# Kernel optimization log

Measured on AMD Instinct MI355X. Metric: run time of the kernel, lower is better.

## Reference

```python
import jax, jax.numpy as jnp
import numpy as np

H, W, V = 32, 64, 13
B, C_IN = 8, 256
RADIUS = 6371.0 * 1000.0
NUM_LAT = H + 2
_j = np.arange(1, NUM_LAT - 1, dtype=np.float64)
_LATS = (90.0 - _j * 180.0 / (NUM_LAT - 1)) * np.pi / 180.0  # [32] radians
PIXEL_X = jnp.asarray(2.0 * np.pi * RADIUS * np.cos(_LATS) / W, dtype=jnp.float32).reshape(1, 1, H, 1)
PIXEL_Y = np.float32(np.pi * RADIUS / (H + 1))
_DZ = np.array([50, 50, 50, 50, 50, 75, 100, 100, 100, 125, 112, 75, 75], dtype=np.float32)
PIXEL_Z = jnp.asarray(_DZ).reshape(1, V, 1, 1)
PRESSURE = jnp.asarray([50, 100, 150, 200, 250, 300, 400, 500, 600, 700, 850, 925, 1000], dtype=jnp.float32).reshape(1, V, 1, 1)
M_Z = jnp.asarray(np.tril(np.ones((V, V), dtype=np.float32)) * _DZ[None, :])  # lower-tri integration matrix
LAT_GRID = jnp.asarray(_LATS, dtype=jnp.float32).reshape(1, 1, H, 1)

OMEGA, L_V, R_GAS, C_P, R_D = 7.29e-5, 2.5e6, 8.314, 1005.0, 287.0
DIFF_RATIO, DT, K_H, K_V = 0.05, 300.0, 15.0, 0.1
SIGMA, EMIS, PTHRESH = 5.67e-8, 0.7, 0.8
sg = jax.lax.stop_gradient


def d_x(f):  # periodic 4th-order diff along W, kernel [1,-8,0,8,-1]/12
    g = (jnp.roll(f, 2, 3) - 8.0 * jnp.roll(f, 1, 3) + 8.0 * jnp.roll(f, -1, 3) - jnp.roll(f, -2, 3)) / 12.0
    return g / PIXEL_X


def d_y(f):  # replicate-block padding along H, kernel [-1,8,0,-8,1]/12
    p = jnp.concatenate([f[:, :, :2], f, f[:, :, -2:]], axis=2)
    g = (-p[:, :, :-4] + 8.0 * p[:, :, 1:-3] - 8.0 * p[:, :, 3:-1] + p[:, :, 4:]) / 12.0
    return g / PIXEL_Y


def d_z(f):  # replicate-block padding along level dim (axis 1)
    p = jnp.concatenate([f[:, :2], f, f[:, -2:]], axis=1)
    g = (-p[:, :-4] + 8.0 * p[:, 1:-3] - 8.0 * p[:, 3:-1] + p[:, 4:]) / 12.0
    return g / PIXEL_Z


def integral_z(f):
    return jnp.einsum('ij,bjhw->bihw', M_Z, f)


def conv3x3(x, w, b):
    y = jax.lax.conv_general_dilated(x, w, (1, 1), ((1, 1), (1, 1)), dimension_numbers=('NCHW', 'OIHW', 'NCHW'))
    return y + b[None, :, None, None]


def batchnorm(x, g, b, eps=1e-5):  # training-mode BN (batch statistics)
    m = x.mean(axis=(0, 2, 3), keepdims=True)
    v = x.var(axis=(0, 2, 3), keepdims=True)
    return (x - m) / jnp.sqrt(v + eps) * g.reshape(1, -1, 1, 1) + b.reshape(1, -1, 1, 1)


def scale_tensor(t, a, b):
    mn, mx = sg(t.min()), sg(t.max())
    return (t - mn) / (mx - mn) * (b - a) + a


def scale_diff(d, x):
    mn, me, mx = sg(x.min()), sg(x.mean()), sg(x.max())
    return scale_tensor(d, (mn - me) * DIFF_RATIO, (mx - me) * DIFF_RATIO)


def avoid_inf(t, thr=1.0):
    t = jnp.where(jnp.abs(t) == 0.0, jnp.full_like(t, 0.1), t)
    return jnp.where(jnp.abs(t) < thr, jnp.sign(t) * thr, t)


def mixing(f):
    return K_H * (d_x(d_x(f)) + d_y(d_y(f))) + K_V * d_z(d_z(f))


def rad_cool(t):
    ta = t + 273.15
    return -(EMIS * SIGMA * ta ** 4) / (C_P * PRESSURE * 100.0 / (R_D * ta))


def saturation(t, z_z):
    rho = -1.0 / avoid_inf(z_z)
    p = rho * R_GAS * t
    tc = t - 273.15
    e_s = 6.112 * jnp.exp(scale_tensor(17.67 * tc / avoid_inf(tc + 243.5), -3.47, 3.01)) * 100.0
    return jnp.maximum(0.622 * e_s / avoid_inf(p - 0.378 * e_s), 1e-6)


def precip(q, q_s):
    rh = q / avoid_inf(q_s)
    rate = (rh > PTHRESH).astype(q.dtype) * (q - PTHRESH * q_s) / DT
    return rate, rate * L_V / C_P


def uv_dt(u, v, w, u_x, v_y, z_x, z_y):
    # u_x, v_y are held fixed across RK stages (stateful self.u_x/self.v_y in the original)
    f_cor = 2.0 * OMEGA * jnp.sin(LAT_GRID)
    u_t = -u * u_x - v * d_y(u) - w * d_z(u) + f_cor * v - z_x + mixing(u)
    v_t = -u * d_x(v) - v * v_y - w * d_z(v) - f_cor * u - z_y + mixing(v)
    return u_t, v_t


def t_dt(u, v, w, t, q, q_s, z_z):
    Q = -L_V * z_z * w
    _, lh = precip(q, q_s)
    return (Q - z_z * w) / C_P - u * d_x(t) - v * d_y(t) - w * d_z(t) + mixing(t) + rad_cool(t) + lh


def pde_forward(x, w_norm, b_norm, w_innorm, b_innorm, coef, gz, bz, gq, bq, gu, bu, gv, bv, gt, bt, gblk, bblk):
    h = conv3x3(x, w_norm, b_norm)  # [B, 65, H, W]
    z, q, u, v, t = jnp.split(h, 5, axis=1)
    z = batchnorm(z, gz, bz); q = batchnorm(q, gq, bq)
    u = batchnorm(u, gu, bu); v = batchnorm(v, gv, bv); t = batchnorm(t, gt, bt)
    z_x, z_y, z_z = d_x(z), d_y(z), d_z(z)
    u_x, v_y = d_x(u), d_y(v)
    w_vel = -integral_z(u_x + v_y)  # continuity: dw/dz = -(u_x + v_y)
    # --- RK4 momentum evolution ---
    k1u, k1v = uv_dt(u, v, w_vel, u_x, v_y, z_x, z_y)
    k2u, k2v = uv_dt(u + 0.5 * DT * k1u, v + 0.5 * DT * k1v, w_vel, u_x, v_y, z_x, z_y)
    k3u, k3v = uv_dt(u + 0.5 * DT * k2u, v + 0.5 * DT * k2v, w_vel, u_x, v_y, z_x, z_y)
    k4u, k4v = uv_dt(u + DT * k3u, v + DT * k3v, w_vel, u_x, v_y, z_x, z_y)
    u_new = u + sg(scale_diff((k1u + 2 * k2u + 2 * k3u + k4u) / 6.0 * DT, u))
    v_new = v + sg(scale_diff((k1v + 2 * k2v + 2 * k3v + k4v) / 6.0 * DT, v))
    # --- RK4 temperature evolution (q_s fixed from initial t) ---
    q_s = saturation(t, z_z)
    k1t = t_dt(u, v, w_vel, t, q, q_s, z_z)
    k2t = t_dt(u, v, w_vel, t + 0.5 * DT * k1t, q, q_s, z_z)
    k3t = t_dt(u, v, w_vel, t + 0.5 * DT * k2t, q, q_s, z_z)
    k4t = t_dt(u, v, w_vel, t + DT * k3t, q, q_s, z_z)
    t_new = t + sg(scale_diff((k1t + 2 * k2t + 2 * k3t + k4t) / 6.0 * DT, t))
    # geopotential tendency uses stateful self.t_t (last computed stage = k4t)
    z_t = integral_z(-R_GAS / PRESSURE * k4t)
    z_new = z + sg(scale_diff(z_t * DT, z))
    # moisture evolution
    pr, _ = precip(q, q_s)
    q_t = -u * d_x(q) - v * d_y(q) - w_vel * d_z(q) + mixing(q) - pr
    q_new = q + sg(scale_diff(q_t * DT, q))
    phys = jnp.concatenate([z_new, q_new, u_new, v_new, t_new], axis=1)
    out = coef * phys + (1.0 - coef) * h
    out = conv3x3(out, w_innorm, b_innorm)
    return batchnorm(out, gblk, bblk) + x


def setup_inputs() -> dict:
    key = jax.random.key(0)
    k0, k1, k2 = jax.random.split(key, 3)
    VD = V * 5
    ones13 = jnp.ones((V,), jnp.float32)
    zeros13 = jnp.zeros((V,), jnp.float32)
    return {
        'x': jax.random.normal(k0, (B, C_IN, H, W), jnp.float32),
        'w_norm': jax.random.normal(k1, (VD, C_IN, 3, 3), jnp.float32) * 0.02,
        'b_norm': jnp.zeros((VD,), jnp.float32),
        'w_innorm': jax.random.normal(k2, (C_IN, VD, 3, 3), jnp.float32) * 0.02,
        'b_innorm': jnp.zeros((C_IN,), jnp.float32),
        'coef': 0.5 * jnp.ones((1, VD, H, W), jnp.float32),
        'gz': 0.1 * ones13, 'bz': zeros13,
        'gq': 0.1 * ones13, 'bq': zeros13,
        'gu': 0.1 * ones13, 'bu': zeros13,
        'gv': 0.1 * ones13, 'bv': zeros13,
        'gt': 0.1 * ones13, 'bt': zeros13,
        'gblk': jnp.ones((C_IN,), jnp.float32),
        'bblk': jnp.zeros((C_IN,), jnp.float32),
    }


def reference(x, w_norm, b_norm, w_innorm, b_innorm, coef, gz, bz, gq, bq, gu, bu, gv, bv, gt, bt, gblk, bblk):
    return pde_forward(x, w_norm, b_norm, w_innorm, b_innorm, coef, gz, bz, gq, bq, gu, bu, gv, bv, gt, bt, gblk, bblk)
```

## Files before the change

kernel.cpp:

```cpp
#include <hip/hip_runtime.h>
#include <math.h>

#define DEVFN static __device__ __forceinline__

static constexpr int BB = 8, VV = 13, HH = 32, WW = 64;
static constexpr int NPLANE = HH * WW;
static constexpr int NF = BB * VV * NPLANE;
static constexpr int NHB = BB * 65 * NPLANE;

static constexpr float DT = 300.0f;
static constexpr float KHc = 15.0f, KVc = 0.1f;
static constexpr float OMEGAc = 7.29e-5f;
static constexpr float L_Vc = 2.5e6f;
static constexpr float R_GASc = 8.314f;
static constexpr float C_Pc = 1005.0f;
static constexpr float PTHc = 0.8f;
static constexpr double PYd = 3.14159265358979323846 * 6371000.0 / 33.0;
static constexpr float PYc  = (float)PYd;
static constexpr float PXCc = (float)(2.0 * 3.14159265358979323846 * 6371000.0 / 64.0);
static constexpr double RCCd = 0.7 * 5.67e-8 * 287.0 / (1005.0 * 100.0);
static constexpr float FBIG = 3.402823466e38f;

__constant__ float cDZ[13]  = {50,50,50,50,50,75,100,100,100,125,112,75,75};
__constant__ float cZI[13] = {
  (float)(1.0/600.0), (float)(1.0/600.0), (float)(1.0/600.0), (float)(1.0/600.0), (float)(1.0/600.0),
  (float)(1.0/900.0), (float)(1.0/1200.0), (float)(1.0/1200.0), (float)(1.0/1200.0),
  (float)(1.0/1500.0), (float)(1.0/1344.0), (float)(1.0/900.0), (float)(1.0/900.0)};
__constant__ float cRC[13] = {
  (float)(-RCCd/50.0), (float)(-RCCd/100.0), (float)(-RCCd/150.0), (float)(-RCCd/200.0),
  (float)(-RCCd/250.0), (float)(-RCCd/300.0), (float)(-RCCd/400.0), (float)(-RCCd/500.0),
  (float)(-RCCd/600.0), (float)(-RCCd/700.0), (float)(-RCCd/850.0), (float)(-RCCd/925.0),
  (float)(-RCCd/1000.0)};
__constant__ float cZW[13] = {
  (float)(50.0*(-8.314/50.0)), (float)(50.0*(-8.314/100.0)), (float)(50.0*(-8.314/150.0)),
  (float)(50.0*(-8.314/200.0)), (float)(50.0*(-8.314/250.0)), (float)(75.0*(-8.314/300.0)),
  (float)(100.0*(-8.314/400.0)), (float)(100.0*(-8.314/500.0)), (float)(100.0*(-8.314/600.0)),
  (float)(125.0*(-8.314/700.0)), (float)(112.0*(-8.314/850.0)), (float)(75.0*(-8.314/925.0)),
  (float)(75.0*(-8.314/1000.0))};

constexpr int pmhC(int r){ return r < 0 ? r + 2 : (r > 31 ? r - 2 : r); }
constexpr int pmvC(int r){ return r < 0 ? r + 2 : (r > 12 ? r - 2 : r); }

struct STab {
  float y1[32][9];
  float y2[32][9];
  float z1[13][9];
  float z2[13][9];
};

constexpr STab makeTab(){
  STab t = {};
  double A[32][32] = {};
  {
    for (int h = 0; h < 32; ++h){
      const double s = 1.0 / 12.0 / PYd;
      A[h][pmhC(h - 2)] += -s;
      A[h][pmhC(h - 1)] +=  8.0 * s;
      A[h][pmhC(h + 1)] += -8.0 * s;
      A[h][pmhC(h + 2)] +=  s;
    }
    for (int h = 0; h < 32; ++h)
      for (int k = 0; k < 9; ++k){
        int c = h - 4 + k;
        if (c >= 0 && c < 32){
          double m = 0.0;
          for (int j = 0; j < 32; ++j) m += A[h][j] * A[j][c];
          t.y2[h][k] = (float)(15.0 * m);
          t.y1[h][k] = (float)A[h][c];
        }
      }
  }
  {
    double dzv[13] = {50,50,50,50,50,75,100,100,100,125,112,75,75};
    double B[13][13] = {};
    for (int v = 0; v < 13; ++v){
      const double s = 1.0 / 12.0 / dzv[v];
      B[v][pmvC(v - 2)] += -s;
      B[v][pmvC(v - 1)] +=  8.0 * s;
      B[v][pmvC(v + 1)] += -8.0 * s;
      B[v][pmvC(v + 2)] +=  s;
    }
    for (int v = 0; v < 13; ++v)
      for (int k = 0; k < 9; ++k){
        int c = v - 4 + k;
        if (c >= 0 && c < 13){
          double m = 0.0;
          for (int j = 0; j < 13; ++j) m += B[v][j] * B[j][c];
          t.z2[v][k] = (float)(0.1 * m);
          t.z1[v][k] = (float)B[v][c];
        }
      }
  }
  return t;
}
__constant__ STab cT = makeTab();

typedef short bf16x8 __attribute__((ext_vector_type(8)));
typedef float f32x4 __attribute__((ext_vector_type(4)));

DEVFN int pmh(int r){ return r < 0 ? r + 2 : (r > HH - 1 ? r - 2 : r); }
DEVFN int pmv(int r){ return r < 0 ? r + 2 : (r > VV - 1 ? r - 2 : r); }
DEVFN float latOf(int h){ return (90.0f - (float)(h + 1) * (180.0f / 33.0f)) * 0.017453292519943295f; }
DEVFN float avoid_inf(float t){
  if (t == 0.0f) t = 0.1f;
  if (fabsf(t) < 1.0f) t = copysignf(1.0f, t);
  return t;
}
DEVFN unsigned short f2bf(float f){
  unsigned u = __float_as_uint(f);
  unsigned r = (u + 0x7fffu + ((u >> 16) & 1u)) >> 16;
  return (unsigned short)r;
}

DEVFN float dxSh(float c0, int w, float invpx){
  float m2 = __shfl(c0, (w + 62) & 63, 64);
  float m1 = __shfl(c0, (w + 63) & 63, 64);
  float p1 = __shfl(c0, (w + 1) & 63, 64);
  float p2 = __shfl(c0, (w + 2) & 63, 64);
  return (m2 - 8.f * m1 + 8.f * p1 - p2) * (1.f / 12.f) * invpx;
}
DEVFN float dxxSh(float c0, int w, float invpx){
  float m4 = __shfl(c0, (w + 60) & 63, 64);
  float m3 = __shfl(c0, (w + 61) & 63, 64);
  float m2 = __shfl(c0, (w + 62) & 63, 64);
  float m1 = __shfl(c0, (w + 63) & 63, 64);
  float p1 = __shfl(c0, (w + 1) & 63, 64);
  float p2 = __shfl(c0, (w + 2) & 63, 64);
  float p3 = __shfl(c0, (w + 3) & 63, 64);
  float p4 = __shfl(c0, (w + 4) & 63, 64);
  float s = m4 - 16.f * m3 + 64.f * m2 + 16.f * m1 - 130.f * c0
          + 16.f * p1 + 64.f * p2 - 16.f * p3 + p4;
  return s * (1.f / 144.f) * invpx * invpx;
}

DEVFN void dyPair(const float* __restrict__ F, const float* __restrict__ c1,
                  const float* __restrict__ c2, int bvbase, int h, int w, float cen,
                  float& dy, float& dyy){
  dy = 0.f; dyy = 0.f;
  #pragma unroll
  for (int k = 0; k < 9; ++k){
    int rr = h - 4 + k; rr = rr < 0 ? 0 : (rr > 31 ? 31 : rr);
    float val = (k == 4) ? cen : F[bvbase + rr * 64 + w];
    dy  = fmaf(c1[k], val, dy);
    dyy = fmaf(c2[k], val, dyy);
  }
}
DEVFN void dzPair(const float* __restrict__ F, const float* __restrict__ c1,
                  const float* __restrict__ c2, int bbase, int v, int hw, float cen,
                  float& dz, float& dzz){
  dz = 0.f; dzz = 0.f;
  #pragma unroll
  for (int k = 0; k < 9; ++k){
    int rr = v - 4 + k; rr = rr < 0 ? 0 : (rr > 12 ? 12 : rr);
    float val = (k == 4) ? cen : F[bbase + rr * 2048 + hw];
    dz  = fmaf(c1[k], val, dz);
    dzz = fmaf(c2[k], val, dzz);
  }
}

DEVFN float waveRedSum(float v){ for (int o = 32; o; o >>= 1) v += __shfl_down(v, o, 64); return v; }
DEVFN float waveRedMin(float v){ for (int o = 32; o; o >>= 1) v = fminf(v, __shfl_down(v, o, 64)); return v; }
DEVFN float waveRedMax(float v){ for (int o = 32; o; o >>= 1) v = fmaxf(v, __shfl_down(v, o, 64)); return v; }

template<int OP, int NWV>
static __device__ float blockRedN(float v){
  __shared__ float s[NWV];
  v = OP == 0 ? waveRedSum(v) : OP == 1 ? waveRedMin(v) : waveRedMax(v);
  int lane = threadIdx.x & 63, wid = threadIdx.x >> 6;
  __syncthreads();
  if (lane == 0) s[wid] = v;
  __syncthreads();
  float r = s[0];
  #pragma unroll
  for (int k = 1; k < NWV; ++k)
    r = OP == 0 ? r + s[k] : OP == 1 ? fminf(r, s[k]) : fmaxf(r, s[k]);
  return r;
}

struct GB { const float* g[5]; const float* b[5]; };

__global__ void __launch_bounds__(256) pre_k(const float* __restrict__ x,
    const float* __restrict__ w1, const float* __restrict__ w2,
    unsigned short* __restrict__ XT, unsigned short* __restrict__ wp1,
    unsigned short* __restrict__ wp2)
{
  int blk = blockIdx.x, t = threadIdx.x;
  if (blk < 1024){
    __shared__ float tile[16 * 68];
    int zz = blk >> 8, rem = blk & 255;
    int b = rem >> 5, h = rem & 31;
    for (int p = zz * 4; p < zz * 4 + 4; ++p){
      int cbase = p * 16;
      __syncthreads();
      {
        int cl = t >> 4, w4 = (t & 15) * 4;
        float4 v = *(const float4*)(x + (((size_t)(b * 256 + cbase + cl) * 32 + h) * 64 + w4));
        tile[cl * 68 + w4 + 0] = v.x; tile[cl * 68 + w4 + 1] = v.y;
        tile[cl * 68 + w4 + 2] = v.z; tile[cl * 68 + w4 + 3] = v.w;
      }
      __syncthreads();
      {
        int w = t >> 2, c4 = (t & 3) * 4;
        ushort4 o;
        o.x = f2bf(tile[(c4 + 0) * 68 + w]);
        o.y = f2bf(tile[(c4 + 1) * 68 + w]);
        o.z = f2bf(tile[(c4 + 2) * 68 + w]);
        o.w = f2bf(tile[(c4 + 3) * 68 + w]);
        *(ushort4*)(XT + (((size_t)(b * 32 + h) * 64 + w) * 256 + cbase + c4)) = o;
      }
    }
  } else {
    const int T1 = 9 * 80 * 256;
    const int T2 = 9 * 256 * 96;
    int idx = (blk - 1024) * 256 + t;
    if (idx < T1){
      int dir = idx / (80 * 256);
      int r = idx - dir * (80 * 256);
      int co = r / 256, ci = r - co * 256;
      float v = (co < 65) ? w1[((size_t)(co * 256 + ci)) * 9 + dir] : 0.f;
      wp1[idx] = f2bf(v);
    } else if (idx < T1 + T2){
      int j = idx - T1;
      int dir = j / (256 * 96);
      int r = j - dir * (256 * 96);
      int co = r / 96, ci = r - co * 96;
      float v = (ci < 65) ? w2[((size_t)(co * 65 + ci)) * 9 + dir] : 0.f;
      wp2[j] = f2bf(v);
    }
  }
}

template<int CIT, int CIL, int CO, int COp, int NW, int MF, int SWZ>
__global__ void __launch_bounds__(NW * 64) conv_mfma_k(
    const unsigned short* __restrict__ XT, const unsigned short* __restrict__ Wp,
    const float* __restrict__ bias, float* __restrict__ out, float* __restrict__ bnp)
{
  __shared__ __align__(16) unsigned short Xl[3 * 34 * CIL];
  const int C8 = CIL / 8;
  int tid = threadIdx.x;
  int bx = blockIdx.x, b = blockIdx.y;
  int h = bx >> 1, p0 = (bx & 1) << 5;
  int bh = b * 64 + bx;
  int wid = tid >> 6, lane = tid & 63;
  int l15 = lane & 15, q = lane >> 4;

  f32x4 acc[MF][2];
  #pragma unroll
  for (int mf = 0; mf < MF; ++mf)
    #pragma unroll
    for (int nf = 0; nf < 2; ++nf){ f32x4 z = {0.f, 0.f, 0.f, 0.f}; acc[mf][nf] = z; }

  for (int cp = 0; cp < CIT / CIL; ++cp){
    if (cp) __syncthreads();
    for (int idx = tid; idx < 3 * 34 * C8; idx += NW * 64){
      int r = idx / (34 * C8);
      int rest = idx - r * (34 * C8);
      int j = rest / C8;
      int c8 = rest - j * C8;
      int hh = h + r - 1;
      int gw = p0 - 1 + j;
      uint4 val = make_uint4(0, 0, 0, 0);
      if (hh >= 0 && hh < 32 && gw >= 0 && gw < 64)
        val = *(const uint4*)(XT + (((size_t)(b * 32 + hh) * 64 + gw) * CIT + cp * CIL + c8 * 8));
      int dst = (r * 34 + j) * CIL + ((c8 * 8) ^ ((j & SWZ) << 3));
      *(uint4*)(Xl + dst) = val;
    }
    __syncthreads();

    for (int dir = 0; dir < 9; ++dir){
      int dy = dir / 3, dx = dir - dy * 3;
      #pragma unroll
      for (int kc = 0; kc < CIL / 32; ++kc){
        int kb = kc * 32 + q * 8;
        bf16x8 a[MF];
        #pragma unroll
        for (int mf = 0; mf < MF; ++mf){
          int co = wid * (MF * 16) + mf * 16 + l15;
          a[mf] = *(const bf16x8*)(Wp + ((size_t)(dir * COp + co) * CIT + cp * CIL + kb));
        }
        #pragma unroll
        for (int nf = 0; nf < 2; ++nf){
          int j = nf * 16 + l15 + dx;
          bf16x8 bfrag = *(const bf16x8*)(Xl + ((dy * 34 + j) * CIL + (kb ^ ((j & SWZ) << 3))));
          #pragma unroll
          for (int mf = 0; mf < MF; ++mf)
            acc[mf][nf] = __builtin_amdgcn_mfma_f32_16x16x32_bf16(a[mf], bfrag, acc[mf][nf], 0, 0, 0);
        }
      }
    }
  }
  #pragma unroll
  for (int mf = 0; mf < MF; ++mf){
    #pragma unroll
    for (int r = 0; r < 4; ++r){
      int co = wid * (MF * 16) + mf * 16 + q * 4 + r;
      if (CO != COp && co >= CO) continue;
      float bv = bias[co];
      float sv = 0.f, sq = 0.f;
      #pragma unroll
      for (int nf = 0; nf < 2; ++nf){
        int pix = nf * 16 + l15;
        float val = acc[mf][nf][r] + bv;
        out[(size_t)(b * CO + co) * 2048 + h * 64 + p0 + pix] = val;
        sv += val; sq += val * val;
      }
      #pragma unroll
      for (int off = 8; off; off >>= 1){
        sv += __shfl_xor(sv, off, 16);
        sq += __shfl_xor(sq, off, 16);
      }
      if (l15 == 0){
        bnp[((size_t)co * 512 + bh) * 2]     = sv;
        bnp[((size_t)co * 512 + bh) * 2 + 1] = sq;
      }
    }
  }
}

__global__ void __launch_bounds__(256) prep_k(const float* __restrict__ hb,
  const float* __restrict__ bnp1, GB gb,
  float* __restrict__ Fz, float* __restrict__ Fq, float* __restrict__ Fu,
  float* __restrict__ Fvf, float* __restrict__ Ft,
  float* __restrict__ zx, float* __restrict__ zy, float* __restrict__ zz,
  float* __restrict__ ux, float* __restrict__ vy, float* __restrict__ wv,
  float* __restrict__ partS)
{
  __shared__ float As[65], Bs[65];
  int blk = blockIdx.x, t = threadIdx.x;
  {
    int wvid = t >> 6, lane = t & 63;
    for (int ch = wvid; ch < 65; ch += 4){
      const float4* pp = (const float4*)(bnp1 + (size_t)ch * 1024) + lane * 4;
      float s = 0.f, sq = 0.f;
      #pragma unroll
      for (int k = 0; k < 4; ++k){ float4 v = pp[k]; s += v.x + v.z; sq += v.y + v.w; }
      s = waveRedSum(s); sq = waveRedSum(sq);
      if (!lane){
        float m = s * (1.f / 16384.f);
        float var = sq * (1.f / 16384.f) - m * m;
        float rstd = rsqrtf(var + 1e-5f);
        int f = ch / 13, k = ch - f * 13;
        float g = gb.g[f][k], bbv = gb.b[f][k];
        As[ch] = g * rstd; Bs[ch] = bbv - m * g * rstd;
      }
    }
  }
  __syncthreads();

  int part = blk >> 6;
  int chunk = blk & 63;
  int b = chunk & 7;
  int p = ((chunk >> 3) << 8) | t;
  int h = p >> 6, w = p & 63;
  int hbase = b * 65 * NPLANE;
  auto hn = [&](int ch, int hh, int ww)->float {
    return hb[hbase + ch * 2048 + hh * 64 + ww] * As[ch] + Bs[ch];
  };
  int fb = (b * 13) * 2048 + p;
  float lat = latOf(h);
  float invpx = 1.0f / (PXCc * cosf(lat));
  int hm2 = pmh(h - 2), hm1 = pmh(h - 1), hp1 = pmh(h + 1), hp2 = pmh(h + 2);
  float fmn = FBIG, fmx = -FBIG, fsm = 0.f, smn = FBIG, smx = -FBIG;
  if (part < 5){
    int ch0 = part * 13;
    float c[13];
    #pragma unroll
    for (int v = 0; v < 13; ++v) c[v] = hn(ch0 + v, h, w);
    float* Fdst = part == 0 ? Fz : part == 1 ? Fq : part == 2 ? Fu : part == 3 ? Fvf : Ft;
    #pragma unroll
    for (int v = 0; v < 13; ++v) Fdst[fb + v * 2048] = c[v];
    if (part == 0){
      #pragma unroll
      for (int v = 0; v < 13; ++v){
        zz[fb + v * 2048] = (-c[pmv(v - 2)] + 8.f * c[pmv(v - 1)] - 8.f * c[pmv(v + 1)] + c[pmv(v + 2)]) * cZI[v];
        float zxv = dxSh(c[v], w, invpx);
        float zyv = (-hn(v, hm2, w) + 8.f * hn(v, hm1, w) - 8.f * hn(v, hp1, w) + hn(v, hp2, w)) * (1.f / 12.f) * (1.f / PYc);
        zx[fb + v * 2048] = zxv; zy[fb + v * 2048] = zyv;
      }
    }
    if (part == 2){
      #pragma unroll
      for (int v = 0; v < 13; ++v)
        ux[fb + v * 2048] = dxSh(c[v], w, invpx);
    }
    if (part == 3){
      #pragma unroll
      for (int v = 0; v < 13; ++v){
        float vyv = (-hn(39 + v, hm2, w) + 8.f * hn(39 + v, hm1, w) - 8.f * hn(39 + v, hp1, w) + hn(39 + v, hp2, w)) * (1.f / 12.f) * (1.f / PYc);
        vy[fb + v * 2048] = vyv;
      }
    }
    if (part == 4){
      #pragma unroll
      for (int v = 0; v < 13; ++v){
        float tcc = c[v] - 273.15f;
        float arg = 17.67f * tcc / avoid_inf(tcc + 243.5f);
        smn = fminf(smn, arg); smx = fmaxf(smx, arg);
      }
    }
    #pragma unroll
    for (int v = 0; v < 13; ++v){ fmn = fminf(fmn, c[v]); fmx = fmaxf(fmx, c[v]); fsm += c[v]; }
  } else {
    float cum = 0.f;
    #pragma unroll
    for (int v = 0; v < 13; ++v){
      float uc = hn(26 + v, h, w);
      float uxv = dxSh(uc, w, invpx);
      float vyv = (-hn(39 + v, hm2, w) + 8.f * hn(39 + v, hm1, w) - 8.f * hn(39 + v, hp1, w) + hn(39 + v, hp2, w)) * (1.f / 12.f) * (1.f / PYc);
      cum += cDZ[v] * (uxv + vyv);
      wv[fb + v * 2048] = -cum;
    }
  }
  float* pb = partS + blk * 17;
  float r;
  r = blockRedN<1,4>(smn); if (!t) pb[0] = r;
  r = blockRedN<2,4>(smx); if (!t) pb[1] = r;
  #pragma unroll
  for (int f = 0; f < 5; ++f){
    r = blockRedN<1,4>(part == f ? fmn : FBIG);  if (!t) pb[2 + f * 3] = r;
    r = blockRedN<2,4>(part == f ? fmx : -FBIG); if (!t) pb[3 + f * 3] = r;
    r = blockRedN<0,4>(part == f ? fsm : 0.f);   if (!t) pb[4 + f * 3] = r;
  }
}

template<int STAGE>
__global__ void __launch_bounds__(256) stage_k(
  const float* __restrict__ U, const float* __restrict__ Vf, const float* __restrict__ T,
  const float* __restrict__ Fu, const float* __restrict__ Fvf, const float* __restrict__ Ft,
  const float* __restrict__ Fq,
  const float* __restrict__ ux, const float* __restrict__ vy,
  const float* __restrict__ zx, const float* __restrict__ zy,
  const float* __restrict__ wv, const float* __restrict__ zz,
  const float* __restrict__ partS,
  float* C0, float* prr,
  float* Uo, float* Vo, float* To,
  float* duA, float* dvA, float* dtA, float* k4t, float* qtA,
  float* pduv, float* pdt, float* pqt, float cnext)
{
  float ss = 0.f, off = 0.f;
  if (STAGE == 1){
    int tt = threadIdx.x;
    float v0 = partS[tt * 17], v1 = partS[tt * 17 + 1];
    if (tt < 128){
      v0 = fminf(v0, partS[(tt + 256) * 17]);
      v1 = fmaxf(v1, partS[(tt + 256) * 17 + 1]);
    }
    float smn = blockRedN<1,4>(v0);
    float smx = blockRedN<2,4>(v1);
    ss = (3.01f + 3.47f) / (smx - smn);
    off = -3.47f - smn * ss;
  }
  int blk = blockIdx.x, t = threadIdx.x;
  int b = blk & 7;
  int rest = blk >> 3;
  int v = rest % 13;
  int hg = rest / 13;
  int h = (hg << 2) | (t >> 6);
  int w = t & 63;
  int bv = b * 13 + v;
  int bvbase = bv * 2048;
  int bbase = b * 13 * 2048;
  int hw = h * 64 + w;
  int i = bvbase + hw;
  float lat = latOf(h);
  float invpx = 1.0f / (PXCc * cosf(lat));
  float fcor = 2.0f * OMEGAc * sinf(lat);
  float wvi = wv[i];
  float Ui = U[i], Vi = Vf[i], Ti = T[i];
  float Fui = (STAGE == 1) ? Ui : Fu[i];
  float Fvi = (STAGE == 1) ? Vi : Fvf[i];

  const float* y1 = cT.y1[h];
  const float* y2 = cT.y2[h];
  const float* z1 = cT.z1[v];
  const float* z2 = cT.z2[v];

  float dyU, dyyU, dzU, dzzU;
  dyPair(U, y1, y2, bvbase, h, w, Ui, dyU, dyyU);
  dzPair(U, z1, z2, bbase, v, hw, Ui, dzU, dzzU);
  float mixU = KHc * dxxSh(Ui, w, invpx) + dyyU + dzzU;
  float ku = -Ui * ux[i] - Vi * dyU - wvi * dzU + fcor * Vi - zx[i] + mixU;

  float dyVd, dyyV, dzV, dzzV;
  dyPair(Vf, y1, y2, bvbase, h, w, Vi, dyVd, dyyV);
  dzPair(Vf, z1, z2, bbase, v, hw, Vi, dzV, dzzV);
  float dxV = dxSh(Vi, w, invpx);
  float mixV = KHc * dxxSh(Vi, w, invpx) + dyyV + dzzV;
  float kv = -Ui * dxV - Vi * vy[i] - wvi * dzV - fcor * Ui - zy[i] + mixV;

  float C0i;
  if (STAGE == 1){
    float zzi = zz[i], qi = Fq[i];
    float rho = -1.0f / avoid_inf(zzi);
    float p = rho * R_GASc * Ti;
    float tcc = Ti - 273.15f;
    float arg = 17.67f * tcc / avoid_inf(tcc + 243.5f);
    float es = 6.112f * expf(arg * ss + off) * 100.0f;
    float qs = fmaxf(0.622f * es / avoid_inf(p - 0.378f * es), 1e-6f);
    float rh = qi / avoid_inf(qs);
    float rate = (rh > PTHc) ? (qi - PTHc * qs) * (1.0f / DT) : 0.0f;
    prr[i] = rate;
    C0i = -(L_Vc + 1.0f) * zzi * wvi * (1.0f / C_Pc) + rate * (L_Vc / C_Pc);
    C0[i] = C0i;
  } else {
    C0i = C0[i];
  }

  float dyT, dyyT, dzT, dzzT;
  dyPair(T, y1, y2, bvbase, h, w, Ti, dyT, dyyT);
  dzPair(T, z1, z2, bbase, v, hw, Ti, dzT, dzzT);
  float dxT = dxSh(Ti, w, invpx);
  float mixT = KHc * dxxSh(Ti, w, invpx) + dyyT + dzzT;
  float ta = Ti + 273.15f;
  float t2 = ta * ta;
  float ta5 = t2 * t2 * ta;
  float rc = cRC[v] * ta5;
  float kt = C0i - Fui * dxT - Fvi * dyT - wvi * dzT + mixT + rc;

  if (STAGE == 1){ duA[i] = ku; dvA[i] = kv; dtA[i] = kt; }
  else if (STAGE < 4){ duA[i] += 2.f * ku; dvA[i] += 2.f * kv; dtA[i] += 2.f * kt; }
  else {
    float au = duA[i] + ku, av = dvA[i] + kv, at = dtA[i] + kt;
    duA[i] = au; dvA[i] = av; dtA[i] = at; k4t[i] = kt;
    float m0 = blockRedN<1,4>(au), m1 = blockRedN<2,4>(au);
    float m2 = blockRedN<1,4>(av), m3 = blockRedN<2,4>(av);
    float m4 = blockRedN<1,4>(at), m5 = blockRedN<2,4>(at);
    if (!t){
      float* pp = pduv + blk * 4;
      pp[0] = m0; pp[1] = m1; pp[2] = m2; pp[3] = m3;
      pdt[blk * 2] = m4; pdt[blk * 2 + 1] = m5;
    }
  }
  if (STAGE < 4){
    float Fti = (STAGE == 1) ? Ti : Ft[i];
    Uo[i] = Fui + cnext * ku;
    Vo[i] = Fvi + cnext * kv;
    To[i] = Fti + cnext * kt;
  }

  if (STAGE == 2){
    float Qc = Fq[i];
    float dyQ, dyyQ, dzQ, dzzQ;
    dyPair(Fq, y1, y2, bvbase, h, w, Qc, dyQ, dyyQ);
    dzPair(Fq, z1, z2, bbase, v, hw, Qc, dzQ, dzzQ);
    float mixQ = KHc * dxxSh(Qc, w, invpx) + dyyQ + dzzQ;
    float qtv = -Fui * dxSh(Qc, w, invpx) - Fvi * dyQ - wvi * dzQ + mixQ - prr[i];
    qtA[i] = qtv;
    float m0 = blockRedN<1,4>(qtv), m1 = blockRedN<2,4>(qtv);
    if (!t){ pqt[blk * 2] = m0; pqt[blk * 2 + 1] = m1; }
  }
}

__global__ void __launch_bounds__(64) zt_k(const float* __restrict__ k4t, float* __restrict__ zt, float* __restrict__ pmm)
{
  int blk = blockIdx.x;
  int b = blk & 7;
  int p = ((blk >> 3) << 6) + threadIdx.x;
  int fb = b * 13 * 2048 + p;
  float cum = 0.f, mn = FBIG, mx = -FBIG;
  #pragma unroll
  for (int v = 0; v < 13; ++v){
    cum += cZW[v] * k4t[fb + v * 2048];
    zt[fb + v * 2048] = cum;
    mn = fminf(mn, cum); mx = fmaxf(mx, cum);
  }
  mn = waveRedMin(mn); mx = waveRedMax(mx);
  if (!threadIdx.x){ pmm[blk * 2] = mn; pmm[blk * 2 + 1] = mx; }
}

__global__ void __launch_bounds__(256) outmid_fused_k(
  const float* __restrict__ hb,
  const float* __restrict__ Fz, const float* __restrict__ Fq, const float* __restrict__ Fu,
  const float* __restrict__ Fvf, const float* __restrict__ Ft,
  const float* __restrict__ ztA, const float* __restrict__ qtA,
  const float* __restrict__ duA, const float* __restrict__ dvA, const float* __restrict__ dtA,
  const float* __restrict__ coef, const float* __restrict__ partS,
  const float* __restrict__ pduv, const float* __restrict__ pdt,
  const float* __restrict__ pqt, const float* __restrict__ pzt,
  unsigned short* __restrict__ MT)
{
  __shared__ float tileBig[65 * 66];
  int blk = blockIdx.x, t = threadIdx.x;

  float fmn[5] = {FBIG, FBIG, FBIG, FBIG, FBIG};
  float fmx[5] = {-FBIG, -FBIG, -FBIG, -FBIG, -FBIG};
  float fsm[5] = {0.f, 0.f, 0.f, 0.f, 0.f};
  #pragma unroll 1
  for (int r0 = t; r0 < 384; r0 += 256){
    const float* pr = partS + r0 * 17;
    #pragma unroll
    for (int f = 0; f < 5; ++f){
      fmn[f] = fminf(fmn[f], pr[2 + f * 3]);
      fmx[f] = fmaxf(fmx[f], pr[3 + f * 3]);
      fsm[f] += pr[4 + f * 3];
    }
  }
  #pragma unroll
  for (int f = 0; f < 5; ++f){
    fmn[f] = blockRedN<1,4>(fmn[f]);
    fmx[f] = blockRedN<2,4>(fmx[f]);
    fsm[f] = blockRedN<0,4>(fsm[f]);
  }
  float dumn = FBIG, dumx = -FBIG, dvmn = FBIG, dvmx = -FBIG, dtmn = FBIG, dtmx = -FBIG;
  float qmn = FBIG, qmx = -FBIG;
  #pragma unroll 1
  for (int r0 = t; r0 < 832; r0 += 256){
    dumn = fminf(dumn, pduv[r0 * 4]);     dumx = fmaxf(dumx, pduv[r0 * 4 + 1]);
    dvmn = fminf(dvmn, pduv[r0 * 4 + 2]); dvmx = fmaxf(dvmx, pduv[r0 * 4 + 3]);
    dtmn = fminf(dtmn, pdt[r0 * 2]);      dtmx = fmaxf(dtmx, pdt[r0 * 2 + 1]);
    qmn = fminf(qmn, pqt[r0 * 2]);        qmx = fmaxf(qmx, pqt[r0 * 2 + 1]);
  }
  float zmn = pzt[t * 2], zmx = pzt[t * 2 + 1];
  dumn = blockRedN<1,4>(dumn); dumx = blockRedN<2,4>(dumx);
  dvmn = blockRedN<1,4>(dvmn); dvmx = blockRedN<2,4>(dvmx);
  dtmn = blockRedN<1,4>(dtmn); dtmx = blockRedN<2,4>(dtmx);
  qmn = blockRedN<1,4>(qmn);   qmx = blockRedN<2,4>(qmx);
  zmn = blockRedN<1,4>(zmn);   zmx = blockRedN<2,4>(zmx);

  float scf[5], off2[5];
  {
    float rmn[5] = {zmn, qmn, dumn, dvmn, dtmn};
    float rmx[5] = {zmx, qmx, dumx, dvmx, dtmx};
    float cfs[5] = {DT, DT, DT / 6.f, DT / 6.f, DT / 6.f};
    #pragma unroll
    for (int f = 0; f < 5; ++f){
      float mnf = fmn[f], mef = fsm[f] * (1.0f / (float)NF), mxf = fmx[f];
      float aa = (mnf - mef) * 0.05f, b2 = (mxf - mef) * 0.05f;
      float cf = cfs[f];
      float dmn = rmn[f] * cf, dmx = rmx[f] * cf;
      float s = (b2 - aa) / (dmx - dmn);
      scf[f] = s * cf; off2[f] = aa - dmn * s;
    }
  }

  int b = blk & 7, h = blk >> 3;
  #pragma unroll 1
  for (int idx = t; idx < 65 * 64; idx += 256){
    int c = idx >> 6, w = idx & 63;
    int f = c / 13, v = c - f * 13;
    int fi = (b * 13 + v) * 2048 + h * 64 + w;
    const float *Fp, *Rp;
    switch (f){
      case 0: Fp = Fz;  Rp = ztA; break;
      case 1: Fp = Fq;  Rp = qtA; break;
      case 2: Fp = Fu;  Rp = duA; break;
      case 3: Fp = Fvf; Rp = dvA; break;
      default: Fp = Ft; Rp = dtA; break;
    }
    float phys = Fp[fi] + Rp[fi] * scf[f] + off2[f];
    float cf = coef[c * 2048 + h * 64 + w];
    float hbv = hb[((size_t)(b * 65 + c)) * 2048 + h * 64 + w];
    tileBig[c * 66 + w] = cf * phys + (1.0f - cf) * hbv;
  }
  __syncthreads();
  #pragma unroll 1
  for (int ph = 0; ph < 6; ++ph){
    int cbase = ph * 16;
    int w = t >> 2, c4 = (t & 3) * 4;
    int c0 = cbase + c4;
    ushort4 o;
    o.x = (c0 + 0 < 65) ? f2bf(tileBig[(c0 + 0) * 66 + w]) : (unsigned short)0;
    o.y = (c0 + 1 < 65) ? f2bf(tileBig[(c0 + 1) * 66 + w]) : (unsigned short)0;
    o.z = (c0 + 2 < 65) ? f2bf(tileBig[(c0 + 2) * 66 + w]) : (unsigned short)0;
    o.w = (c0 + 3 < 65) ? f2bf(tileBig[(c0 + 3) * 66 + w]) : (unsigned short)0;
    *(ushort4*)(MT + (((size_t)(b * 32 + h) * 64 + w) * 96 + c0)) = o;
  }
}

__global__ void __launch_bounds__(256) final_k(float* __restrict__ y, const float* __restrict__ x,
  const float* __restrict__ bnp2, const float* __restrict__ gblk, const float* __restrict__ bblk)
{
  int blk = blockIdx.x, t = threadIdx.x;
  int c = (blk >> 1) & 255;
  float4 pv = ((const float4*)(bnp2 + (size_t)c * 1024))[t];
  float s = pv.x + pv.z, sq = pv.y + pv.w;
  s = blockRedN<0,4>(s); sq = blockRedN<0,4>(sq);
  float m = s * (1.0f / 16384.0f);
  float var = sq * (1.0f / 16384.0f) - m * m;
  float rstd = rsqrtf(var + 1e-5f);
  float a = gblk[c] * rstd, bb = bblk[c] - m * gblk[c] * rstd;
  int e4 = blk * 256 + t;
  float4 v = ((const float4*)y)[e4];
  float4 xv = ((const float4*)x)[e4];
  v.x = v.x * a + bb + xv.x;
  v.y = v.y * a + bb + xv.y;
  v.z = v.z * a + bb + xv.z;
  v.w = v.w * a + bb + xv.w;
  ((float4*)y)[e4] = v;
}

extern "C" void kernel_launch(void* const* d_in, const int* in_sizes, int n_in,
                              void* d_out, int out_size, void* d_ws, size_t ws_size,
                              hipStream_t stream)
{
  (void)in_sizes; (void)n_in; (void)out_size; (void)ws_size;
  const float* x        = (const float*)d_in[0];
  const float* w_norm   = (const float*)d_in[1];
  const float* b_norm   = (const float*)d_in[2];
  const float* w_innorm = (const float*)d_in[3];
  const float* b_innorm = (const float*)d_in[4];
  const float* coef     = (const float*)d_in[5];
  GB gb;
  for (int f = 0; f < 5; ++f){
    gb.g[f] = (const float*)d_in[6 + 2 * f];
    gb.b[f] = (const float*)d_in[7 + 2 * f];
  }
  const float* gblk = (const float*)d_in[16];
  const float* bblk = (const float*)d_in[17];
  float* yout = (float*)d_out;

  float* ws = (float*)d_ws;
  size_t off = 0;
  auto alloc = [&](size_t n){ float* p = ws + off; off += n; return p; };
  float* hb  = alloc(NHB);
  float* Fz  = alloc(NF); float* Fq  = alloc(NF); float* Fu  = alloc(NF);
  float* Fvf = alloc(NF); float* Ft  = alloc(NF);
  float* zx  = alloc(NF); float* zy  = alloc(NF); float* zz  = alloc(NF);
  float* ux  = alloc(NF); float* vy  = alloc(NF); float* wvel = alloc(NF);
  float* C0  = alloc(NF); float* prr = alloc(NF);
  float* Ua  = alloc(NF); float* Ub  = alloc(NF); float* Va  = alloc(NF); float* Vb = alloc(NF);
  float* Ta  = alloc(NF); float* Tb  = alloc(NF);
  float* duA = alloc(NF); float* dvA = alloc(NF); float* dtA = alloc(NF);
  float* k4t = alloc(NF); float* ztA = alloc(NF); float* qtA = alloc(NF);
  float* part1 = alloc(384 * 17 + 4);
  float* pduv = alloc(832 * 4); float* pdt = alloc(832 * 2);
  float* pqt  = alloc(832 * 2); float* pzt = alloc(256 * 2);
  float* bnp1 = alloc(65 * 512 * 2);
  float* bnp2 = alloc(256 * 512 * 2);
  float* Wp1f = alloc(9 * 80 * 256 / 2);
  float* Wp2f = alloc(9 * 256 * 96 / 2);
  unsigned short* Wp1 = (unsigned short*)Wp1f;
  unsigned short* Wp2 = (unsigned short*)Wp2f;
  unsigned short* XT = (unsigned short*)Ua;
  unsigned short* MT = (unsigned short*)C0;

  pre_k<<<2608, 256, 0, stream>>>(x, w_norm, w_innorm, XT, Wp1, Wp2);
  conv_mfma_k<256, 128, 65, 80, 5, 1, 7><<<dim3(64, 8), 5 * 64, 0, stream>>>(XT, Wp1, b_norm, hb, bnp1);
  prep_k<<<384, 256, 0, stream>>>(hb, bnp1, gb, Fz, Fq, Fu, Fvf, Ft, zx, zy, zz, ux, vy, wvel, part1);
  stage_k<1><<<NF / 256, 256, 0, stream>>>(Fu, Fvf, Ft, Fu, Fvf, Ft, Fq, ux, vy, zx, zy, wvel, zz, part1,
      C0, prr, Ua, Va, Ta, duA, dvA, dtA, k4t, qtA, pduv, pdt, pqt, 0.5f * DT);
  stage_k<2><<<NF / 256, 256, 0, stream>>>(Ua, Va, Ta, Fu, Fvf, Ft, Fq, ux, vy, zx, zy, wvel, zz, part1,
      C0, prr, Ub, Vb, Tb, duA, dvA, dtA, k4t, qtA, pduv, pdt, pqt, 0.5f * DT);
  stage_k<3><<<NF / 256, 256, 0, stream>>>(Ub, Vb, Tb, Fu, Fvf, Ft, Fq, ux, vy, zx, zy, wvel, zz, part1,
      C0, prr, Ua, Va, Ta, duA, dvA, dtA, k4t, qtA, pduv, pdt, pqt, DT);
  stage_k<4><<<NF / 256, 256, 0, stream>>>(Ua, Va, Ta, Fu, Fvf, Ft, Fq, ux, vy, zx, zy, wvel, zz, part1,
      C0, prr, Ub, Vb, Tb, duA, dvA, dtA, k4t, qtA, pduv, pdt, pqt, 0.f);
  zt_k<<<256, 64, 0, stream>>>(k4t, ztA, pzt);
  outmid_fused_k<<<256, 256, 0, stream>>>(hb, Fz, Fq, Fu, Fvf, Ft, ztA, qtA, duA, dvA, dtA,
      coef, part1, pduv, pdt, pqt, pzt, MT);
  conv_mfma_k<96, 96, 256, 256, 8, 2, 3><<<dim3(64, 8), 8 * 64, 0, stream>>>(MT, Wp2, b_innorm, yout, bnp2);
  final_k<<<4096, 256, 0, stream>>>(yout, x, bnp2, gblk, bblk);
}
```

Baseline: 153.3 us.

## Interleave U/V/T and per-point fields into float4 arrays for stage kernels

Packs the prognostic fields U, V, T into one float4 array, and likewise packs the forcing copies, the precomputed derivative fields, the C0/rate/wvel/zz fields and the RK accumulators into float4 arrays. Each stencil tap in the stage kernels then fetches all three variables with a single 16-byte load instead of three separate scalar loads. This cuts load instruction count and improves coalescing in the memory-bound RK stages. In exchange it wastes a padding lane in several arrays, so more bytes move per point, and prep_k now writes strided scattered stores.

Result: slower. 158.1 us (+3.1%).

```diff
diff --git a/kernel.cpp b/kernel.cpp
--- a/kernel.cpp
+++ b/kernel.cpp
@@ -131,31 +131,6 @@
   float s = m4 - 16.f * m3 + 64.f * m2 + 16.f * m1 - 130.f * c0
           + 16.f * p1 + 64.f * p2 - 16.f * p3 + p4;
   return s * (1.f / 144.f) * invpx * invpx;
-}
-
-DEVFN void dyPair(const float* __restrict__ F, const float* __restrict__ c1,
-                  const float* __restrict__ c2, int bvbase, int h, int w, float cen,
-                  float& dy, float& dyy){
-  dy = 0.f; dyy = 0.f;
-  #pragma unroll
-  for (int k = 0; k < 9; ++k){
-    int rr = h - 4 + k; rr = rr < 0 ? 0 : (rr > 31 ? 31 : rr);
-    float val = (k == 4) ? cen : F[bvbase + rr * 64 + w];
-    dy  = fmaf(c1[k], val, dy);
-    dyy = fmaf(c2[k], val, dyy);
-  }
-}
-DEVFN void dzPair(const float* __restrict__ F, const float* __restrict__ c1,
-                  const float* __restrict__ c2, int bbase, int v, int hw, float cen,
-                  float& dz, float& dzz){
-  dz = 0.f; dzz = 0.f;
-  #pragma unroll
-  for (int k = 0; k < 9; ++k){
-    int rr = v - 4 + k; rr = rr < 0 ? 0 : (rr > 12 ? 12 : rr);
-    float val = (k == 4) ? cen : F[bbase + rr * 2048 + hw];
-    dz  = fmaf(c1[k], val, dz);
-    dzz = fmaf(c2[k], val, dzz);
-  }
 }
 
 DEVFN float waveRedSum(float v){ for (int o = 32; o; o >>= 1) v += __shfl_down(v, o, 64); return v; }
@@ -321,8 +296,8 @@
   const float* __restrict__ bnp1, GB gb,
   float* __restrict__ Fz, float* __restrict__ Fq, float* __restrict__ Fu,
   float* __restrict__ Fvf, float* __restrict__ Ft,
-  float* __restrict__ zx, float* __restrict__ zy, float* __restrict__ zz,
-  float* __restrict__ ux, float* __restrict__ vy, float* __restrict__ wv,
+  float* __restrict__ D0f, float* __restrict__ F4f,
+  float* __restrict__ S1f, float* __restrict__ S2f,
   float* __restrict__ partS)
 {
   __shared__ float As[65], Bs[65];
@@ -372,27 +347,44 @@
     if (part == 0){
       #pragma unroll
       for (int v = 0; v < 13; ++v){
-        zz[fb + v * 2048] = (-c[pmv(v - 2)] + 8.f * c[pmv(v - 1)] - 8.f * c[pmv(v + 1)] + c[pmv(v + 2)]) * cZI[v];
+        int idx = fb + v * 2048;
+        S2f[(size_t)idx * 4 + 1] = (-c[pmv(v - 2)] + 8.f * c[pmv(v - 1)] - 8.f * c[pmv(v + 1)] + c[pmv(v + 2)]) * cZI[v];
         float zxv = dxSh(c[v], w, invpx);
         float zyv = (-hn(v, hm2, w) + 8.f * hn(v, hm1, w) - 8.f * hn(v, hp1, w) + hn(v, hp2, w)) * (1.f / 12.f) * (1.f / PYc);
-        zx[fb + v * 2048] = zxv; zy[fb + v * 2048] = zyv;
-      }
+        S1f[(size_t)idx * 4 + 2] = zxv;
+        S1f[(size_t)idx * 4 + 3] = zyv;
+      }
+    }
+    if (part == 1){
+      #pragma unroll
+      for (int v = 0; v < 13; ++v)
+        F4f[(size_t)(fb + v * 2048) * 4 + 3] = c[v];
     }
     if (part == 2){
       #pragma unroll
-      for (int v = 0; v < 13; ++v)
-        ux[fb + v * 2048] = dxSh(c[v], w, invpx);
+      for (int v = 0; v < 13; ++v){
+        int idx = fb + v * 2048;
+        S1f[(size_t)idx * 4 + 0] = dxSh(c[v], w, invpx);
+        F4f[(size_t)idx * 4 + 0] = c[v];
+        D0f[(size_t)idx * 4 + 0] = c[v];
+      }
     }
     if (part == 3){
       #pragma unroll
       for (int v = 0; v < 13; ++v){
+        int idx = fb + v * 2048;
         float vyv = (-hn(39 + v, hm2, w) + 8.f * hn(39 + v, hm1, w) - 8.f * hn(39 + v, hp1, w) + hn(39 + v, hp2, w)) * (1.f / 12.f) * (1.f / PYc);
-        vy[fb + v * 2048] = vyv;
+        S1f[(size_t)idx * 4 + 1] = vyv;
+        F4f[(size_t)idx * 4 + 1] = c[v];
+        D0f[(size_t)idx * 4 + 1] = c[v];
       }
     }
     if (part == 4){
       #pragma unroll
       for (int v = 0; v < 13; ++v){
+        int idx = fb + v * 2048;
+        F4f[(size_t)idx * 4 + 2] = c[v];
+        D0f[(size_t)idx * 4 + 2] = c[v];
         float tcc = c[v] - 273.15f;
         float arg = 17.67f * tcc / avoid_inf(tcc + 243.5f);
         smn = fminf(smn, arg); smx = fmaxf(smx, arg);
@@ -408,7 +400,7 @@
       float uxv = dxSh(uc, w, invpx);
       float vyv = (-hn(39 + v, hm2, w) + 8.f * hn(39 + v, hm1, w) - 8.f * hn(39 + v, hp1, w) + hn(39 + v, hp2, w)) * (1.f / 12.f) * (1.f / PYc);
       cum += cDZ[v] * (uxv + vyv);
-      wv[fb + v * 2048] = -cum;
+      S2f[(size_t)(fb + v * 2048) * 4 + 0] = -cum;
     }
   }
   float* pb = partS + blk * 17;
@@ -425,16 +417,12 @@
 
 template<int STAGE>
 __global__ void __launch_bounds__(256) stage_k(
-  const float* __restrict__ U, const float* __restrict__ Vf, const float* __restrict__ T,
-  const float* __restrict__ Fu, const float* __restrict__ Fvf, const float* __restrict__ Ft,
-  const float* __restrict__ Fq,
-  const float* __restrict__ ux, const float* __restrict__ vy,
-  const float* __restrict__ zx, const float* __restrict__ zy,
-  const float* __restrict__ wv, const float* __restrict__ zz,
-  const float* __restrict__ partS,
-  float* C0, float* prr,
-  float* Uo, float* Vo, float* To,
-  float* duA, float* dvA, float* dtA, float* k4t, float* qtA,
+  const float4* __restrict__ D, const float4* __restrict__ F4,
+  const float4* __restrict__ S1, float4* __restrict__ S2,
+  const float* __restrict__ Fq, const float* __restrict__ partS,
+  float4* __restrict__ Dn, float4* __restrict__ A,
+  float* __restrict__ duA, float* __restrict__ dvA, float* __restrict__ dtA,
+  float* __restrict__ k4t, float* __restrict__ qtA,
   float* pduv, float* pdt, float* pqt, float cnext)
 {
   float ss = 0.f, off = 0.f;
@@ -465,32 +453,50 @@
   float lat = latOf(h);
   float invpx = 1.0f / (PXCc * cosf(lat));
   float fcor = 2.0f * OMEGAc * sinf(lat);
-  float wvi = wv[i];
-  float Ui = U[i], Vi = Vf[i], Ti = T[i];
-  float Fui = (STAGE == 1) ? Ui : Fu[i];
-  float Fvi = (STAGE == 1) ? Vi : Fvf[i];
+
+  float4 Di = D[i];
+  float Ui = Di.x, Vi = Di.y, Ti = Di.z;
+  float4 s1 = S1[i];
+  float4 s2 = S2[i];
+  float wvi = s2.x;
+  float Fui, Fvi, Fti;
+  if (STAGE == 1){ Fui = Ui; Fvi = Vi; Fti = Ti; }
+  else { float4 f4 = F4[i]; Fui = f4.x; Fvi = f4.y; Fti = f4.z; }
 
   const float* y1 = cT.y1[h];
   const float* y2 = cT.y2[h];
   const float* z1 = cT.z1[v];
   const float* z2 = cT.z2[v];
 
-  float dyU, dyyU, dzU, dzzU;
-  dyPair(U, y1, y2, bvbase, h, w, Ui, dyU, dyyU);
-  dzPair(U, z1, z2, bbase, v, hw, Ui, dzU, dzzU);
+  float dyU = 0.f, dyyU = 0.f, dyV = 0.f, dyyV = 0.f, dyT = 0.f, dyyT = 0.f;
+  #pragma unroll
+  for (int k = 0; k < 9; ++k){
+    int rr = h - 4 + k; rr = rr < 0 ? 0 : (rr > 31 ? 31 : rr);
+    float4 val = (k == 4) ? Di : D[bvbase + rr * 64 + w];
+    dyU = fmaf(y1[k], val.x, dyU); dyyU = fmaf(y2[k], val.x, dyyU);
+    dyV = fmaf(y1[k], val.y, dyV); dyyV = fmaf(y2[k], val.y, dyyV);
+    dyT = fmaf(y1[k], val.z, dyT); dyyT = fmaf(y2[k], val.z, dyyT);
+  }
+  float dzU = 0.f, dzzU = 0.f, dzV = 0.f, dzzV = 0.f, dzT = 0.f, dzzT = 0.f;
+  #pragma unroll
+  for (int k = 0; k < 9; ++k){
+    int rr = v - 4 + k; rr = rr < 0 ? 0 : (rr > 12 ? 12 : rr);
+    float4 val = (k == 4) ? Di : D[bbase + rr * 2048 + hw];
+    dzU = fmaf(z1[k], val.x, dzU); dzzU = fmaf(z2[k], val.x, dzzU);
+    dzV = fmaf(z1[k], val.y, dzV); dzzV = fmaf(z2[k], val.y, dzzV);
+    dzT = fmaf(z1[k], val.z, dzT); dzzT = fmaf(z2[k], val.z, dzzT);
+  }
+
   float mixU = KHc * dxxSh(Ui, w, invpx) + dyyU + dzzU;
-  float ku = -Ui * ux[i] - Vi * dyU - wvi * dzU + fcor * Vi - zx[i] + mixU;
-
-  float dyVd, dyyV, dzV, dzzV;
-  dyPair(Vf, y1, y2, bvbase, h, w, Vi, dyVd, dyyV);
-  dzPair(Vf, z1, z2, bbase, v, hw, Vi, dzV, dzzV);
+  float ku = -Ui * s1.x - Vi * dyU - wvi * dzU + fcor * Vi - s1.z + mixU;
+
   float dxV = dxSh(Vi, w, invpx);
   float mixV = KHc * dxxSh(Vi, w, invpx) + dyyV + dzzV;
-  float kv = -Ui * dxV - Vi * vy[i] - wvi * dzV - fcor * Ui - zy[i] + mixV;
-
-  float C0i;
+  float kv = -Ui * dxV - Vi * s1.y - wvi * dzV - fcor * Ui - s1.w + mixV;
+
+  float C0i, rate = 0.f;
   if (STAGE == 1){
-    float zzi = zz[i], qi = Fq[i];
+    float zzi = s2.y, qi = Fq[i];
     float rho = -1.0f / avoid_inf(zzi);
     float p = rho * R_GASc * Ti;
     float tcc = Ti - 273.15f;
@@ -498,17 +504,13 @@
     float es = 6.112f * expf(arg * ss + off) * 100.0f;
     float qs = fmaxf(0.622f * es / avoid_inf(p - 0.378f * es), 1e-6f);
     float rh = qi / avoid_inf(qs);
-    float rate = (rh > PTHc) ? (qi - PTHc * qs) * (1.0f / DT) : 0.0f;
-    prr[i] = rate;
+    rate = (rh > PTHc) ? (qi - PTHc * qs) * (1.0f / DT) : 0.0f;
     C0i = -(L_Vc + 1.0f) * zzi * wvi * (1.0f / C_Pc) + rate * (L_Vc / C_Pc);
-    C0[i] = C0i;
+    *(float2*)((float*)&S2[i] + 2) = make_float2(C0i, rate);
   } else {
-    C0i = C0[i];
-  }
-
-  float dyT, dyyT, dzT, dzzT;
-  dyPair(T, y1, y2, bvbase, h, w, Ti, dyT, dyyT);
-  dzPair(T, z1, z2, bbase, v, hw, Ti, dzT, dzzT);
+    C0i = s2.z;
+  }
+
   float dxT = dxSh(Ti, w, invpx);
   float mixT = KHc * dxxSh(Ti, w, invpx) + dyyT + dzzT;
   float ta = Ti + 273.15f;
@@ -517,10 +519,15 @@
   float rc = cRC[v] * ta5;
   float kt = C0i - Fui * dxT - Fvi * dyT - wvi * dzT + mixT + rc;
 
-  if (STAGE == 1){ duA[i] = ku; dvA[i] = kv; dtA[i] = kt; }
-  else if (STAGE < 4){ duA[i] += 2.f * ku; dvA[i] += 2.f * kv; dtA[i] += 2.f * kt; }
-  else {
-    float au = duA[i] + ku, av = dvA[i] + kv, at = dtA[i] + kt;
+  if (STAGE == 1){
+    A[i] = make_float4(ku, kv, kt, 0.f);
+  } else if (STAGE < 4){
+    float4 a = A[i];
+    a.x += 2.f * ku; a.y += 2.f * kv; a.z += 2.f * kt;
+    A[i] = a;
+  } else {
+    float4 a = A[i];
+    float au = a.x + ku, av = a.y + kv, at = a.z + kt;
     duA[i] = au; dvA[i] = av; dtA[i] = at; k4t[i] = kt;
     float m0 = blockRedN<1,4>(au), m1 = blockRedN<2,4>(au);
     float m2 = blockRedN<1,4>(av), m3 = blockRedN<2,4>(av);
@@ -531,20 +538,26 @@
       pdt[blk * 2] = m4; pdt[blk * 2 + 1] = m5;
     }
   }
-  if (STAGE < 4){
-    float Fti = (STAGE == 1) ? Ti : Ft[i];
-    Uo[i] = Fui + cnext * ku;
-    Vo[i] = Fvi + cnext * kv;
-    To[i] = Fti + cnext * kt;
-  }
+  if (STAGE < 4)
+    Dn[i] = make_float4(Fui + cnext * ku, Fvi + cnext * kv, Fti + cnext * kt, 0.f);
 
   if (STAGE == 2){
     float Qc = Fq[i];
-    float dyQ, dyyQ, dzQ, dzzQ;
-    dyPair(Fq, y1, y2, bvbase, h, w, Qc, dyQ, dyyQ);
-    dzPair(Fq, z1, z2, bbase, v, hw, Qc, dzQ, dzzQ);
+    float dyQ = 0.f, dyyQ = 0.f, dzQ = 0.f, dzzQ = 0.f;
+    #pragma unroll
+    for (int k = 0; k < 9; ++k){
+      int rr = h - 4 + k; rr = rr < 0 ? 0 : (rr > 31 ? 31 : rr);
+      float val = (k == 4) ? Qc : Fq[bvbase + rr * 64 + w];
+      dyQ = fmaf(y1[k], val, dyQ); dyyQ = fmaf(y2[k], val, dyyQ);
+    }
+    #pragma unroll
+    for (int k = 0; k < 9; ++k){
+      int rr = v - 4 + k; rr = rr < 0 ? 0 : (rr > 12 ? 12 : rr);
+      float val = (k == 4) ? Qc : Fq[bbase + rr * 2048 + hw];
+      dzQ = fmaf(z1[k], val, dzQ); dzzQ = fmaf(z2[k], val, dzzQ);
+    }
     float mixQ = KHc * dxxSh(Qc, w, invpx) + dyyQ + dzzQ;
-    float qtv = -Fui * dxSh(Qc, w, invpx) - Fvi * dyQ - wvi * dzQ + mixQ - prr[i];
+    float qtv = -Fui * dxSh(Qc, w, invpx) - Fvi * dyQ - wvi * dzQ + mixQ - s2.w;
     qtA[i] = qtv;
     float m0 = blockRedN<1,4>(qtv), m1 = blockRedN<2,4>(qtv);
     if (!t){ pqt[blk * 2] = m0; pqt[blk * 2 + 1] = m1; }
@@ -712,14 +725,15 @@
   float* ws = (float*)d_ws;
   size_t off = 0;
   auto alloc = [&](size_t n){ float* p = ws + off; off += n; return p; };
+  float* Daf = alloc((size_t)NF * 4);
+  float* Dbf = alloc((size_t)NF * 4);
+  float* Af  = alloc((size_t)NF * 4);
+  float* F4f = alloc((size_t)NF * 4);
+  float* S1f = alloc((size_t)NF * 4);
+  float* S2f = alloc((size_t)NF * 4);
   float* hb  = alloc(NHB);
   float* Fz  = alloc(NF); float* Fq  = alloc(NF); float* Fu  = alloc(NF);
   float* Fvf = alloc(NF); float* Ft  = alloc(NF);
-  float* zx  = alloc(NF); float* zy  = alloc(NF); float* zz  = alloc(NF);
-  float* ux  = alloc(NF); float* vy  = alloc(NF); float* wvel = alloc(NF);
-  float* C0  = alloc(NF); float* prr = alloc(NF);
-  float* Ua  = alloc(NF); float* Ub  = alloc(NF); float* Va  = alloc(NF); float* Vb = alloc(NF);
-  float* Ta  = alloc(NF); float* Tb  = alloc(NF);
   float* duA = alloc(NF); float* dvA = alloc(NF); float* dtA = alloc(NF);
   float* k4t = alloc(NF); float* ztA = alloc(NF); float* qtA = alloc(NF);
   float* part1 = alloc(384 * 17 + 4);
@@ -731,20 +745,24 @@
   float* Wp2f = alloc(9 * 256 * 96 / 2);
   unsigned short* Wp1 = (unsigned short*)Wp1f;
   unsigned short* Wp2 = (unsigned short*)Wp2f;
-  unsigned short* XT = (unsigned short*)Ua;
-  unsigned short* MT = (unsigned short*)C0;
+  unsigned short* XT = (unsigned short*)Daf;
+  unsigned short* MT = (unsigned short*)S2f;
+
+  float4* Da = (float4*)Daf; float4* Db = (float4*)Dbf;
+  float4* A4 = (float4*)Af;  float4* F4 = (float4*)F4f;
+  float4* S1 = (float4*)S1f; float4* S2 = (float4*)S2f;
 
   pre_k<<<2608, 256, 0, stream>>>(x, w_norm, w_innorm, XT, Wp1, Wp2);
   conv_mfma_k<256, 128, 65, 80, 5, 1, 7><<<dim3(64, 8), 5 * 64, 0, stream>>>(XT, Wp1, b_norm, hb, bnp1);
-  prep_k<<<384, 256, 0, stream>>>(hb, bnp1, gb, Fz, Fq, Fu, Fvf, Ft, zx, zy, zz, ux, vy, wvel, part1);
-  stage_k<1><<<NF / 256, 256, 0, stream>>>(Fu, Fvf, Ft, Fu, Fvf, Ft, Fq, ux, vy, zx, zy, wvel, zz, part1,
-      C0, prr, Ua, Va, Ta, duA, dvA, dtA, k4t, qtA, pduv, pdt, pqt, 0.5f * DT);
-  stage_k<2><<<NF / 256, 256, 0, stream>>>(Ua, Va, Ta, Fu, Fvf, Ft, Fq, ux, vy, zx, zy, wvel, zz, part1,
-      C0, prr, Ub, Vb, Tb, duA, dvA, dtA, k4t, qtA, pduv, pdt, pqt, 0.5f * DT);
-  stage_k<3><<<NF / 256, 256, 0, stream>>>(Ub, Vb, Tb, Fu, Fvf, Ft, Fq, ux, vy, zx, zy, wvel, zz, part1,
-      C0, prr, Ua, Va, Ta, duA, dvA, dtA, k4t, qtA, pduv, pdt, pqt, DT);
-  stage_k<4><<<NF / 256, 256, 0, stream>>>(Ua, Va, Ta, Fu, Fvf, Ft, Fq, ux, vy, zx, zy, wvel, zz, part1,
-      C0, prr, Ub, Vb, Tb, duA, dvA, dtA, k4t, qtA, pduv, pdt, pqt, 0.f);
+  prep_k<<<384, 256, 0, stream>>>(hb, bnp1, gb, Fz, Fq, Fu, Fvf, Ft, Daf, F4f, S1f, S2f, part1);
+  stage_k<1><<<NF / 256, 256, 0, stream>>>(Da, F4, S1, S2, Fq, part1, Db, A4,
+      duA, dvA, dtA, k4t, qtA, pduv, pdt, pqt, 0.5f * DT);
+  stage_k<2><<<NF / 256, 256, 0, stream>>>(Db, F4, S1, S2, Fq, part1, Da, A4,
+      duA, dvA, dtA, k4t, qtA, pduv, pdt, pqt, 0.5f * DT);
+  stage_k<3><<<NF / 256, 256, 0, stream>>>(Da, F4, S1, S2, Fq, part1, Db, A4,
+      duA, dvA, dtA, k4t, qtA, pduv, pdt, pqt, DT);
+  stage_k<4><<<NF / 256, 256, 0, stream>>>(Db, F4, S1, S2, Fq, part1, Da, A4,
+      duA, dvA, dtA, k4t, qtA, pduv, pdt, pqt, 0.f);
   zt_k<<<256, 64, 0, stream>>>(k4t, ztA, pzt);
   outmid_fused_k<<<256, 256, 0, stream>>>(hb, Fz, Fq, Fu, Fvf, Ft, ztA, qtA, duA, dvA, dtA,
       coef, part1, pduv, pdt, pqt, pzt, MT);
```
